# Kernel tuning notes

Hardware: AMD Instinct MI355X
Metric: run time of the kernel (lower is better)

The kernel has to match this reference:

```python
import jax, jax.numpy as jnp
import numpy as np

NUM_USERS = 100000
NUM_BOOKS = 50000
N_NODES = NUM_USERS + NUM_BOOKS
LATENT = 64
NUM_LAYERS = 3
N_EDGES = 2400000


def setup_inputs() -> dict:
    key = jax.random.key(0)
    ks = jax.random.split(key, 12)
    edge_index = jax.random.randint(ks[0], (2, N_EDGES), 0, N_NODES)
    embedding = jax.random.normal(ks[1], (N_NODES, LATENT), dtype=jnp.float32) * 0.1
    user_features = jax.random.normal(ks[2], (NUM_USERS, 16), dtype=jnp.float32)
    book_numerical_features = jax.random.normal(ks[3], (NUM_BOOKS, 8), dtype=jnp.float32)
    book_genre_features = jax.random.normal(ks[4], (NUM_BOOKS, 32), dtype=jnp.float32)
    W_user = jax.random.normal(ks[5], (16, LATENT), dtype=jnp.float32) * 0.1
    b_user = jnp.zeros((LATENT,), dtype=jnp.float32)
    W_num = jax.random.normal(ks[6], (8, LATENT), dtype=jnp.float32) * 0.1
    b_num = jnp.zeros((LATENT,), dtype=jnp.float32)
    W_genre = jax.random.normal(ks[7], (32, LATENT), dtype=jnp.float32) * 0.1
    b_genre = jnp.zeros((LATENT,), dtype=jnp.float32)
    return {
        "edge_index": edge_index,
        "embedding": embedding,
        "user_features": user_features,
        "book_numerical_features": book_numerical_features,
        "book_genre_features": book_genre_features,
        "W_user": W_user, "b_user": b_user,
        "W_num": W_num, "b_num": b_num,
        "W_genre": W_genre, "b_genre": b_genre,
    }


def reference(edge_index, embedding, user_features, book_numerical_features,
              book_genre_features, W_user, b_user, W_num, b_num, W_genre, b_genre):
    N = embedding.shape[0]
    # feature projections fused into initial embedding (emb0)
    user_proj = user_features @ W_user + b_user                       # [Nu, D]
    book_proj = (book_numerical_features @ W_num + b_num
                 + book_genre_features @ W_genre + b_genre)           # [Nb, D]
    emb0 = embedding + jnp.concatenate([user_proj, book_proj], axis=0)  # [N, D]

    frm, to = edge_index[0], edge_index[1]
    # symmetric degree normalization: deg counts incoming edges at target nodes
    deg = jax.ops.segment_sum(jnp.ones_like(to, dtype=emb0.dtype), to, num_segments=N)
    deg_inv_sqrt = jnp.where(deg > 0, deg ** -0.5, 0.0)
    norm = deg_inv_sqrt[frm] * deg_inv_sqrt[to]                       # [E]

    # LightGCN: gather -> scale -> scatter-add, then mean over all layer outputs
    emb = emb0
    acc = emb0
    for _ in range(NUM_LAYERS):
        msg = norm[:, None] * emb[frm]                                # [E, D]
        emb = jax.ops.segment_sum(msg, to, num_segments=N)            # [N, D]
        acc = acc + emb
    out = acc / (NUM_LAYERS + 1)
    return emb0, out
```

## Files before the change

kernel.cpp:

```cpp
#include <hip/hip_runtime.h>
#include <hip/hip_bf16.h>

typedef __hip_bfloat16 bf16;

#define D 64
#define BSH 8
#define CAP 5120
#define EPB 4096
#define NPW 8


__global__ __launch_bounds__(256) void k_initcur(int* __restrict__ gcur, int nbk) {
    int i = blockIdx.x * 256 + threadIdx.x;
    if (i < nbk) gcur[i] = i * CAP;
}


__global__ __launch_bounds__(256) void k_part(const int* __restrict__ frm,
                                              const int* __restrict__ to,
                                              int* __restrict__ gcur,
                                              int* __restrict__ be, int E, int nbk) {
    __shared__ int h[1024];
    int tid = threadIdx.x;
    for (int i = tid; i < 1024; i += 256) h[i] = 0;
    __syncthreads();

    int base = blockIdx.x * EPB;
    int  f[16], bk[16], tl[16];
    bool va[16];
    #pragma unroll
    for (int k = 0; k < 16; k++) {
        int i = base + k * 256 + tid;
        va[k] = (i < E);
        int ic = va[k] ? i : 0;
        int t = to[ic];
        f[k]  = frm[ic];
        bk[k] = t >> BSH;
        tl[k] = t & 255;
        if (va[k]) atomicAdd(&h[bk[k]], 1);
    }
    __syncthreads();
    for (int b = tid; b < nbk; b += 256) {
        int c = h[b];
        h[b] = (c > 0) ? atomicAdd(&gcur[b], c) : 0;
    }
    __syncthreads();
    #pragma unroll
    for (int k = 0; k < 16; k++) {
        if (va[k]) {
            int pos = atomicAdd(&h[bk[k]], 1);
            be[pos] = (f[k] << 8) | tl[k];
        }
    }
}


__global__ void k_bscan(const int* __restrict__ gcur, int* __restrict__ bstart,
                        int* __restrict__ row_start, int nbk, int N, int E) {
    __shared__ int s[1024];
    int t = threadIdx.x;
    int x = (t < nbk) ? (gcur[t] - t * CAP) : 0;
    s[t] = x;
    __syncthreads();
    #pragma unroll
    for (int off = 1; off < 1024; off <<= 1) {
        int v = s[t] + ((t >= off) ? s[t - off] : 0);
        __syncthreads();
        s[t] = v;
        __syncthreads();
    }
    if (t < nbk) bstart[t] = s[t] - x;
    if (t == 0) row_start[N] = E;
}


__global__ __launch_bounds__(256) void k_scatter(const int* __restrict__ gcur,
                                                 const int* __restrict__ bstart,
                                                 const int* __restrict__ be,
                                                 int* __restrict__ row_start,
                                                 float* __restrict__ dis,
                                                 int* __restrict__ csr, int N) {
    __shared__ int hist[256];
    __shared__ int scn[256];
    int b = blockIdx.x;
    int t = threadIdx.x;
    hist[t] = 0;
    __syncthreads();

    int base = b * CAP;
    int cnt  = gcur[b] - base;
    for (int i = t; i < cnt; i += 256)
        atomicAdd(&hist[be[base + i] & 255], 1);
    __syncthreads();

    int d = hist[t];
    scn[t] = d;
    __syncthreads();
    #pragma unroll
    for (int off = 1; off < 256; off <<= 1) {
        int v = scn[t] + ((t >= off) ? scn[t - off] : 0);
        __syncthreads();
        scn[t] = v;
        __syncthreads();
    }
    int rs = bstart[b] + (scn[t] - d);

    int node = (b << BSH) + t;
    if (node < N) {
        row_start[node] = rs;
        dis[node] = (d > 0) ? rsqrtf((float)d) : 0.0f;
    }
    hist[t] = rs;
    __syncthreads();

    for (int i = t; i < cnt; i += 256) {
        int rec = be[base + i];
        int pos = atomicAdd(&hist[rec & 255], 1);
        csr[pos] = rec >> 8;
    }
}


__global__ __launch_bounds__(256) void k_emb0(const float* __restrict__ emb,
                       const float* __restrict__ uf,
                       const float* __restrict__ bn,
                       const float* __restrict__ bg,
                       const float* __restrict__ Wu,
                       const float* __restrict__ bu,
                       const float* __restrict__ Wn,
                       const float* __restrict__ bnb,
                       const float* __restrict__ Wg,
                       const float* __restrict__ bgb,
                       const float* __restrict__ dis,
                       float* __restrict__ out0, bf16* __restrict__ y0,
                       int N, int NU, int ublocks) {
    int lane = threadIdx.x & 63;
    int wsub = __builtin_amdgcn_readfirstlane(threadIdx.x >> 6);

    if (blockIdx.x < ublocks) {
        float w[16];
        #pragma unroll
        for (int k = 0; k < 16; k++) w[k] = Wu[k * D + lane];
        float bias = bu[lane];

        int node0 = (blockIdx.x * 4 + wsub) * NPW;
        for (int n = 0; n < NPW; n++) {
            int node = node0 + n;
            if (node >= NU) break;
            const float4* f = (const float4*)(uf + (size_t)node * 16);
            float4 f0 = f[0], f1 = f[1], f2 = f[2], f3 = f[3];
            float p = bias
                + f0.x * w[0]  + f0.y * w[1]  + f0.z * w[2]  + f0.w * w[3]
                + f1.x * w[4]  + f1.y * w[5]  + f1.z * w[6]  + f1.w * w[7]
                + f2.x * w[8]  + f2.y * w[9]  + f2.z * w[10] + f2.w * w[11]
                + f3.x * w[12] + f3.y * w[13] + f3.z * w[14] + f3.w * w[15];
            size_t idx = (size_t)node * D + lane;
            float v = emb[idx] + p;
            out0[idx] = v;
            y0[idx]   = __float2bfloat16(dis[node] * v);
        }
    } else {
        float wn[8], wg[32];
        #pragma unroll
        for (int k = 0; k < 8; k++)  wn[k] = Wn[k * D + lane];
        #pragma unroll
        for (int k = 0; k < 32; k++) wg[k] = Wg[k * D + lane];
        float bias = bnb[lane] + bgb[lane];

        int b0 = ((blockIdx.x - ublocks) * 4 + wsub) * NPW;
        for (int n = 0; n < NPW; n++) {
            int b = b0 + n;
            int node = NU + b;
            if (node >= N) break;
            const float4* fn = (const float4*)(bn + (size_t)b * 8);
            float4 n0 = fn[0], n1 = fn[1];
            const float4* fg = (const float4*)(bg + (size_t)b * 32);
            float p = bias
                + n0.x * wn[0] + n0.y * wn[1] + n0.z * wn[2] + n0.w * wn[3]
                + n1.x * wn[4] + n1.y * wn[5] + n1.z * wn[6] + n1.w * wn[7];
            #pragma unroll
            for (int q = 0; q < 8; q++) {
                float4 g = fg[q];
                p += g.x * wg[4*q]   + g.y * wg[4*q+1]
                   + g.z * wg[4*q+2] + g.w * wg[4*q+3];
            }
            size_t idx = (size_t)node * D + lane;
            float v = emb[idx] + p;
            out0[idx] = v;
            y0[idx]   = __float2bfloat16(dis[node] * v);
        }
    }
}


static __device__ __forceinline__ unsigned int pack_bf16x2(float e, float o) {
    bf16 a = __float2bfloat16(e);
    bf16 b = __float2bfloat16(o);
    unsigned short ua = __builtin_bit_cast(unsigned short, a);
    unsigned short ub = __builtin_bit_cast(unsigned short, b);
    return (unsigned int)ua | ((unsigned int)ub << 16);
}


static __device__ __forceinline__ void gather4(
        const int* __restrict__ row_start, const int* __restrict__ csr,
        const unsigned int* __restrict__ y32, int n0, int N, int lane,
        float (&a0)[4], float (&a1)[4]) {
    int half = lane >> 5;
    int lh   = lane & 31;
    int l16  = lane & 15;

    int sv[4], ev[4];
    #pragma unroll
    for (int g = 0; g < 4; g++) {
        int node = min(n0 + g, N - 1);
        sv[g] = row_start[node];
        ev[g] = row_start[node + 1];
        a0[g] = 0.f;
        a1[g] = 0.f;
    }

    for (int c = 0; ; c++) {
        int jv[4], base[4];
        #pragma unroll
        for (int g = 0; g < 4; g++) {
            base[g] = sv[g] + 16 * c;
            jv[g] = csr[min(base[g] + l16, max(ev[g] - 1, 0))];
        }
        #pragma unroll
        for (int u = 0; u < 8; u++) {
            #pragma unroll
            for (int g = 0; g < 4; g++) {
                int idx = 2 * u + half;
                int j = __shfl(jv[g], idx);
                unsigned int d = y32[((unsigned int)j << 5) + lh];
                d = (base[g] + idx < ev[g]) ? d : 0u;
                a0[g] += __uint_as_float(d << 16);
                a1[g] += __uint_as_float(d & 0xffff0000u);
            }
        }
        bool cont = false;
        #pragma unroll
        for (int g = 0; g < 4; g++) cont = cont || (base[g] + 16 < ev[g]);
        if (!cont) break;
    }

    #pragma unroll
    for (int g = 0; g < 4; g++) {
        a0[g] += __shfl_xor(a0[g], 32);
        a1[g] += __shfl_xor(a1[g], 32);
    }
}


__global__ __launch_bounds__(256) void k_prop(const int* __restrict__ row_start,
                       const int* __restrict__ csr,
                       const float* __restrict__ dis,
                       const bf16* __restrict__ y_in,
                       bf16* __restrict__ x_out,
                       bf16* __restrict__ y_out, int N) {
    int lane = threadIdx.x & 63;
    int n0 = (blockIdx.x * 4 + (threadIdx.x >> 6)) * 4;
    if (n0 >= N) return;

    float a0[4], a1[4];
    gather4(row_start, csr, (const unsigned int*)y_in, n0, N, lane, a0, a1);

    int half = lane >> 5;
    int lh   = lane & 31;
    #pragma unroll
    for (int g = 0; g < 4; g++) {
        int node = n0 + g;
        if (node >= N) break;
        float dt = dis[node];
        float x0  = dt * a0[g];
        float x1v = dt * a1[g];
        unsigned int w = (unsigned int)node * 32 + lh;
        if (half == 0) {
            ((unsigned int*)x_out)[w] = pack_bf16x2(x0, x1v);
        } else {
            ((unsigned int*)y_out)[w] = pack_bf16x2(dt * x0, dt * x1v);
        }
    }
}


__global__ __launch_bounds__(256) void k_prop_last(const int* __restrict__ row_start,
                       const int* __restrict__ csr,
                       const float* __restrict__ dis,
                       const bf16* __restrict__ y_in,
                       const float* __restrict__ out0,
                       const bf16* __restrict__ x1,
                       const bf16* __restrict__ x2,
                       float* __restrict__ out1, int N) {
    int lane = threadIdx.x & 63;
    int n0 = (blockIdx.x * 4 + (threadIdx.x >> 6)) * 4;
    if (n0 >= N) return;

    float a0[4], a1[4];
    gather4(row_start, csr, (const unsigned int*)y_in, n0, N, lane, a0, a1);

    int half = lane >> 5;
    int lh   = lane & 31;
    #pragma unroll
    for (int g = 0; g < 4; g++) {
        int node = n0 + g;
        if (node >= N) break;
        float dt = dis[node];
        float x3e = dt * a0[g];
        float x3o = dt * a1[g];
        if (half == 0) {
            unsigned int w = (unsigned int)node * 32 + lh;
            float2 o0 = ((const float2*)out0)[w];
            unsigned int p1 = ((const unsigned int*)x1)[w];
            unsigned int p2 = ((const unsigned int*)x2)[w];
            float e1 = __uint_as_float(p1 << 16);
            float o1 = __uint_as_float(p1 & 0xffff0000u);
            float e2 = __uint_as_float(p2 << 16);
            float o2 = __uint_as_float(p2 & 0xffff0000u);
            float2 r;
            r.x = (o0.x + e1 + e2 + x3e) * 0.25f;
            r.y = (o0.y + o1 + o2 + x3o) * 0.25f;
            ((float2*)out1)[w] = r;
        }
    }
}


extern "C" void kernel_launch(void* const* d_in, const int* in_sizes, int n_in,
                              void* d_out, int out_size, void* d_ws, size_t ws_size,
                              hipStream_t stream) {
    const int E  = in_sizes[0] / 2;
    const int N  = in_sizes[1] / D;
    const int NU = in_sizes[2] / 16;
    const int nbk = (N + 255) >> BSH;

    const int*   frm = (const int*)d_in[0];
    const int*   to  = frm + E;
    const float* emb = (const float*)d_in[1];
    const float* uf  = (const float*)d_in[2];
    const float* bn  = (const float*)d_in[3];
    const float* bg  = (const float*)d_in[4];
    const float* Wu  = (const float*)d_in[5];
    const float* bu  = (const float*)d_in[6];
    const float* Wn  = (const float*)d_in[7];
    const float* bnb = (const float*)d_in[8];
    const float* Wg  = (const float*)d_in[9];
    const float* bgb = (const float*)d_in[10];

    char* p = (char*)d_ws;
    const size_t ND = (size_t)N * D;
    bf16*  y0        = (bf16*)p;   p += ND * sizeof(bf16);
    bf16*  y1        = (bf16*)p;   p += ND * sizeof(bf16);
    bf16*  x1        = (bf16*)p;   p += ND * sizeof(bf16);
    bf16*  x2        = (bf16*)p;   p += ND * sizeof(bf16);
    float* dis       = (float*)p;  p += (size_t)N * sizeof(float);
    int*   row_start = (int*)p;    p += ((size_t)N + 16) * sizeof(int);
    int*   bstart    = (int*)p;    p += 1024 * sizeof(int);
    int*   gcur      = (int*)p;    p += (size_t)nbk * sizeof(int);
    int*   csr       = (int*)p;    p += (size_t)E * sizeof(int);
    int*   be        = (int*)p;    p += (size_t)nbk * CAP * sizeof(int);

    const int TB = 256;
    const int gridProp = (N + 15) / 16;
    const int gridPart = (E + EPB - 1) / EPB;

    k_initcur<<<(nbk + TB - 1) / TB, TB, 0, stream>>>(gcur, nbk);
    k_part   <<<gridPart, TB, 0, stream>>>(frm, to, gcur, be, E, nbk);
    k_bscan  <<<1, 1024, 0, stream>>>(gcur, bstart, row_start, nbk, N, E);
    k_scatter<<<nbk, TB, 0, stream>>>(gcur, bstart, be, row_start, dis, csr, N);

    float* out0 = (float*)d_out;
    float* out1 = out0 + ND;

    const int NB = N - NU;
    const int uwaves  = (NU + NPW - 1) / NPW;
    const int ublocks = (uwaves + 3) / 4;
    const int bwaves  = (NB + NPW - 1) / NPW;
    const int bblocks = (bwaves + 3) / 4;
    k_emb0<<<ublocks + bblocks, TB, 0, stream>>>(emb, uf, bn, bg, Wu, bu, Wn, bnb,
                                                 Wg, bgb, dis, out0, y0, N, NU, ublocks);

    k_prop     <<<gridProp, TB, 0, stream>>>(row_start, csr, dis, y0, x1, y1, N);
    k_prop     <<<gridProp, TB, 0, stream>>>(row_start, csr, dis, y1, x2, y0, N);
    k_prop_last<<<gridProp, TB, 0, stream>>>(row_start, csr, dis, y0, out0, x1, x2, out1, N);
}
```

Baseline: 389.1 us.

## Stage partitioned edges in LDS for coalesced bucket writes, enlarge partition blocks

The partition kernel now handles 16K edges per 1024-thread block. It computes a block-local prefix scan of bucket counts, sorts records into an LDS staging buffer by bucket, and then writes each bucket's run to global memory with one wave per bucket. This replaces the old scattered per-element global writes with contiguous writes and cuts the number of global atomics on bucket cursors. The scatter kernel also moves to 1024 threads per block. The cost is 76KB of LDS per partition block, which lowers occupancy, plus extra scan and sync overhead.

```diff
diff --git a/kernel.cpp b/kernel.cpp
--- a/kernel.cpp
+++ b/kernel.cpp
@@ -6,7 +6,8 @@
 #define D 64
 #define BSH 8
 #define CAP 5120
-#define EPB 4096
+#define EPB 16384
+#define PTB 1024
 #define NPW 8
 
 
@@ -16,13 +17,18 @@
 }
 
 
-__global__ __launch_bounds__(256) void k_part(const int* __restrict__ frm,
-                                              const int* __restrict__ to,
-                                              int* __restrict__ gcur,
-                                              int* __restrict__ be, int E, int nbk) {
-    __shared__ int h[1024];
+__global__ __launch_bounds__(1024) void k_part(const int* __restrict__ frm,
+                                               const int* __restrict__ to,
+                                               int* __restrict__ gcur,
+                                               int* __restrict__ be, int E, int nbk) {
+    __shared__ int hist[1024];
+    __shared__ int lofs[1024];
+    __shared__ int gbase[1024];
+    __shared__ int wsum[16];
+    __shared__ int stage[EPB];
+
     int tid = threadIdx.x;
-    for (int i = tid; i < 1024; i += 256) h[i] = 0;
+    hist[tid] = 0;
     __syncthreads();
 
     int base = blockIdx.x * EPB;
@@ -30,27 +36,58 @@
     bool va[16];
     #pragma unroll
     for (int k = 0; k < 16; k++) {
-        int i = base + k * 256 + tid;
+        int i = base + k * PTB + tid;
         va[k] = (i < E);
-        int ic = va[k] ? i : 0;
+        int ic = va[k] ? i : base;
         int t = to[ic];
         f[k]  = frm[ic];
         bk[k] = t >> BSH;
         tl[k] = t & 255;
-        if (va[k]) atomicAdd(&h[bk[k]], 1);
-    }
-    __syncthreads();
-    for (int b = tid; b < nbk; b += 256) {
-        int c = h[b];
-        h[b] = (c > 0) ? atomicAdd(&gcur[b], c) : 0;
-    }
-    __syncthreads();
+        if (va[k]) atomicAdd(&hist[bk[k]], 1);
+    }
+    __syncthreads();
+
+    int c = hist[tid];
+    int lane = tid & 63, wv = tid >> 6;
+    int x = c;
+    #pragma unroll
+    for (int off = 1; off < 64; off <<= 1) {
+        int y = __shfl_up(x, off);
+        if (lane >= off) x += y;
+    }
+    if (lane == 63) wsum[wv] = x;
+    __syncthreads();
+    if (wv == 0) {
+        int wval = (lane < 16) ? wsum[lane] : 0;
+        #pragma unroll
+        for (int off = 1; off < 16; off <<= 1) {
+            int y = __shfl_up(wval, off);
+            if (lane >= off) wval += y;
+        }
+        if (lane < 16) wsum[lane] = wval;
+    }
+    __syncthreads();
+    int excl = x + (wv ? wsum[wv - 1] : 0) - c;
+    lofs[tid]  = excl;
+    gbase[tid] = (c > 0 && tid < nbk) ? atomicAdd(&gcur[tid], c) : 0;
+    hist[tid]  = excl;
+    __syncthreads();
+
     #pragma unroll
     for (int k = 0; k < 16; k++) {
         if (va[k]) {
-            int pos = atomicAdd(&h[bk[k]], 1);
-            be[pos] = (f[k] << 8) | tl[k];
-        }
+            int p = atomicAdd(&hist[bk[k]], 1);
+            stage[p] = (f[k] << 8) | tl[k];
+        }
+    }
+    __syncthreads();
+
+    for (int b = wv; b < nbk; b += 16) {
+        int ls = lofs[b];
+        int le = hist[b];
+        int gd = gbase[b];
+        for (int i = ls + lane; i < le; i += 64)
+            be[gd + (i - ls)] = stage[i];
     }
 }
 
@@ -74,46 +111,48 @@
 }
 
 
-__global__ __launch_bounds__(256) void k_scatter(const int* __restrict__ gcur,
-                                                 const int* __restrict__ bstart,
-                                                 const int* __restrict__ be,
-                                                 int* __restrict__ row_start,
-                                                 float* __restrict__ dis,
-                                                 int* __restrict__ csr, int N) {
+__global__ __launch_bounds__(1024) void k_scatter(const int* __restrict__ gcur,
+                                                  const int* __restrict__ bstart,
+                                                  const int* __restrict__ be,
+                                                  int* __restrict__ row_start,
+                                                  float* __restrict__ dis,
+                                                  int* __restrict__ csr, int N) {
     __shared__ int hist[256];
     __shared__ int scn[256];
     int b = blockIdx.x;
     int t = threadIdx.x;
-    hist[t] = 0;
+    if (t < 256) hist[t] = 0;
     __syncthreads();
 
     int base = b * CAP;
     int cnt  = gcur[b] - base;
-    for (int i = t; i < cnt; i += 256)
+    for (int i = t; i < cnt; i += PTB)
         atomicAdd(&hist[be[base + i] & 255], 1);
     __syncthreads();
 
-    int d = hist[t];
-    scn[t] = d;
+    int d = 0;
+    if (t < 256) { d = hist[t]; scn[t] = d; }
     __syncthreads();
     #pragma unroll
     for (int off = 1; off < 256; off <<= 1) {
-        int v = scn[t] + ((t >= off) ? scn[t - off] : 0);
+        int v = 0;
+        if (t < 256) v = scn[t] + ((t >= off) ? scn[t - off] : 0);
         __syncthreads();
-        scn[t] = v;
+        if (t < 256) scn[t] = v;
         __syncthreads();
     }
-    int rs = bstart[b] + (scn[t] - d);
-
-    int node = (b << BSH) + t;
-    if (node < N) {
-        row_start[node] = rs;
-        dis[node] = (d > 0) ? rsqrtf((float)d) : 0.0f;
-    }
-    hist[t] = rs;
-    __syncthreads();
-
-    for (int i = t; i < cnt; i += 256) {
+    if (t < 256) {
+        int rs = bstart[b] + (scn[t] - d);
+        int node = (b << BSH) + t;
+        if (node < N) {
+            row_start[node] = rs;
+            dis[node] = (d > 0) ? rsqrtf((float)d) : 0.0f;
+        }
+        hist[t] = rs;
+    }
+    __syncthreads();
+
+    for (int i = t; i < cnt; i += PTB) {
         int rec = be[base + i];
         int pos = atomicAdd(&hist[rec & 255], 1);
         csr[pos] = rec >> 8;
@@ -366,9 +405,9 @@
     const int gridPart = (E + EPB - 1) / EPB;
 
     k_initcur<<<(nbk + TB - 1) / TB, TB, 0, stream>>>(gcur, nbk);
-    k_part   <<<gridPart, TB, 0, stream>>>(frm, to, gcur, be, E, nbk);
+    k_part   <<<gridPart, PTB, 0, stream>>>(frm, to, gcur, be, E, nbk);
     k_bscan  <<<1, 1024, 0, stream>>>(gcur, bstart, row_start, nbk, N, E);
-    k_scatter<<<nbk, TB, 0, stream>>>(gcur, bstart, be, row_start, dis, csr, N);
+    k_scatter<<<nbk, PTB, 0, stream>>>(gcur, bstart, be, row_start, dis, csr, N);
 
     float* out0 = (float*)d_out;
     float* out1 = out0 + ND;
```

After: 378.9 us. 1.03x faster.
